# Kernel optimization log

Hardware: AMD Instinct MI355X
Metric: run time of the kernel (lower is better)

## Reference

```python
import jax, jax.numpy as jnp
import numpy as np

S = 2        # downscale
REDUCE = 32  # QK channel dim


def _to_grid(x):
    # [B,C,H,W] -> [B,C,H/S,W/S,S*S], matching ConverToGrid (reshape+permute+reshape)
    B, C, H, W = x.shape
    h, w = H // S, W // S
    x = x.reshape(B, C, h, S, w, S)
    x = x.transpose(0, 1, 2, 4, 3, 5)
    return x.reshape(B, C, h, w, S * S)


def setup_inputs() -> dict:
    key = jax.random.key(0)
    k1, k2, k3 = jax.random.split(key, 3)
    fm = jax.random.normal(k1, (8, 128, 256, 256), dtype=jnp.float32)
    Wq = jax.random.normal(k2, (REDUCE, 128), dtype=jnp.float32) * 0.05
    Wk = jax.random.normal(k3, (REDUCE, 128), dtype=jnp.float32) * 0.05
    return {"fm": fm, "Wq": Wq, "Wk": Wk}


def reference(fm, Wq, Wk):
    B, C, H, W = fm.shape
    h, w = H // S, W // S
    # Q branch: AvgPool2d(S,S) -> 1x1 conv -> scale by 1/sqrt(reduce)
    pooled = fm.reshape(B, C, h, S, w, S).mean(axis=(3, 5))          # [B,C,h,w]
    Q = jnp.einsum('rc,bchw->brhw', Wq, pooled) / jnp.sqrt(
        jnp.asarray(REDUCE, fm.dtype))                               # [B,r,h,w]
    # K branch: 1x1 conv -> grid
    K = _to_grid(jnp.einsum('rc,bchw->brhw', Wk, fm))                # [B,r,h,w,S*S]
    # V branch: grid of raw features
    V = _to_grid(fm)                                                 # [B,C,h,w,S*S]
    # sum over channel dim of Q*K, softmax over window dim (dropout p=0 => identity)
    logits = jnp.einsum('brhw,brhws->bhws', Q, K)                    # [B,h,w,S*S]
    attn = jax.nn.softmax(logits, axis=-1)
    # weighted sum over window positions
    out = jnp.einsum('bchws,bhws->bchw', V, attn)                    # [B,C,h,w]
    return out
```

## Files before the change

kernel.cpp:

```cpp
#include <hip/hip_runtime.h>
#include <hip/hip_bf16.h>
#include <math.h>


typedef unsigned int uint32;

__device__ __forceinline__ uint32 pack2(float x, float y) {
  union { __hip_bfloat162 h; uint32 u; } cvt;
  cvt.h = __float22bfloat162_rn(make_float2(x, y));
  return cvt.u;
}
__device__ __forceinline__ float2 unpack2(uint32 u) {
  float2 r;
  r.x = __uint_as_float(u << 16);
  r.y = __uint_as_float(u & 0xffff0000u);
  return r;
}

__global__ __launch_bounds__(256) void wt_kernel(const float* __restrict__ Wq,
                                                 const float* __restrict__ Wk,
                                                 float* __restrict__ ws) {
  int t = blockIdx.x * 256 + threadIdx.x;
  if (t < 4096) {
    int c = t >> 5, r = t & 31;
    ws[c * 32 + r]        = Wq[r * 128 + c] * (0.25f / sqrtf(32.0f));
    ws[4096 + c * 32 + r] = Wk[r * 128 + c];
  }
}

__global__ __launch_bounds__(256)
__attribute__((amdgpu_waves_per_eu(4, 4)))
void attn_main(const float* __restrict__ fm,
               const float* __restrict__ ws,
               float* __restrict__ out) {
  __shared__ float Qpart[2 * 32 * 64];
  __shared__ float lbuf[4 * 64 * 4];

  const int tid = threadIdx.x;
  const int p   = tid & 63;
  const int grp = __builtin_amdgcn_readfirstlane(tid >> 6);

  const int blk = blockIdx.x;
  const int w0  = (blk & 1) * 64;
  const int h   = (blk >> 1) & 127;
  const int b   = blk >> 8;
  const int cb  = grp * 32;

  const float* gbase = fm + ((size_t)(b * 128 + cb) * 65536) +
                       (size_t)(2 * h) * 256 + 2 * (w0 + p);
  const float* wq = ws + cb * 32;
  const float* wk = ws + 4096 + cb * 32;

  uint32 pka[32], pkb[32];
  {
    const float* g = gbase;
#pragma unroll
    for (int i = 0; i < 32; ++i) {
      const float2 va = *(const float2*)(g);
      const float2 vb = *(const float2*)(g + 256);
      pka[i] = pack2(va.x, va.y);
      pkb[i] = pack2(vb.x, vb.y);
      g += 65536;
    }
  }

  float qa[32];
#pragma unroll
  for (int r = 0; r < 32; ++r) qa[r] = 0.f;
#pragma unroll
  for (int i = 0; i < 32; ++i) {
    const float2 va = unpack2(pka[i]);
    const float2 vb = unpack2(pkb[i]);
    const float u = (va.x + va.y) + (vb.x + vb.y);
#pragma unroll
    for (int r = 0; r < 32; ++r)
      qa[r] = fmaf(wq[i * 32 + r], u, qa[r]);
  }

  if (grp >= 2) {
#pragma unroll
    for (int r = 0; r < 32; ++r) Qpart[(grp - 2) * 2048 + r * 64 + p] = qa[r];
  }
  __syncthreads();
  if (grp < 2) {
#pragma unroll
    for (int r = 0; r < 32; ++r) Qpart[grp * 2048 + r * 64 + p] += qa[r];
  }
  __syncthreads();
#pragma unroll
  for (int r = 0; r < 32; ++r)
    qa[r] = Qpart[r * 64 + p] + Qpart[2048 + r * 64 + p];

  float l0 = 0.f, l1 = 0.f, l2 = 0.f, l3 = 0.f;
#pragma unroll
  for (int i = 0; i < 32; ++i) {
    const float2 va = unpack2(pka[i]);
    const float2 vb = unpack2(pkb[i]);
    float t0 = 0.f, t1 = 0.f;
#pragma unroll
    for (int r = 0; r < 32; r += 2) {
      t0 = fmaf(qa[r + 0], wk[i * 32 + r + 0], t0);
      t1 = fmaf(qa[r + 1], wk[i * 32 + r + 1], t1);
    }
    const float tv = t0 + t1;
    l0 = fmaf(tv, va.x, l0);
    l1 = fmaf(tv, va.y, l1);
    l2 = fmaf(tv, vb.x, l2);
    l3 = fmaf(tv, vb.y, l3);
  }
  *(float4*)(lbuf + (grp * 64 + p) * 4) = make_float4(l0, l1, l2, l3);
  __syncthreads();

  if (grp == 0) {
    const float4 o1 = *(const float4*)(lbuf + (64 + p) * 4);
    const float4 o2 = *(const float4*)(lbuf + (128 + p) * 4);
    const float4 o3 = *(const float4*)(lbuf + (192 + p) * 4);
    const float L0 = (l0 + o1.x) + (o2.x + o3.x);
    const float L1 = (l1 + o1.y) + (o2.y + o3.y);
    const float L2 = (l2 + o1.z) + (o2.z + o3.z);
    const float L3 = (l3 + o1.w) + (o2.w + o3.w);
    const float mx = fmaxf(fmaxf(L0, L1), fmaxf(L2, L3));
    const float e0 = __expf(L0 - mx), e1 = __expf(L1 - mx);
    const float e2 = __expf(L2 - mx), e3 = __expf(L3 - mx);
    const float inv = 1.0f / ((e0 + e1) + (e2 + e3));
    *(float4*)(lbuf + p * 4) =
        make_float4(e0 * inv, e1 * inv, e2 * inv, e3 * inv);
  }
  __syncthreads();
  const float4 at = *(const float4*)(lbuf + p * 4);

  {
    float* op = out + ((size_t)(b * 128 + cb) * 16384) + h * 128 + w0 + p;
#pragma unroll
    for (int i = 0; i < 32; ++i) {
      const float2 va = unpack2(pka[i]);
      const float2 vb = unpack2(pkb[i]);
      op[(size_t)i * 16384] =
          fmaf(at.x, va.x, fmaf(at.y, va.y, fmaf(at.z, vb.x, at.w * vb.y)));
    }
  }
}

extern "C" void kernel_launch(void* const* d_in, const int* in_sizes, int n_in,
                              void* d_out, int out_size, void* d_ws, size_t ws_size,
                              hipStream_t stream) {
  const float* fm = (const float*)d_in[0];
  const float* Wq = (const float*)d_in[1];
  const float* Wk = (const float*)d_in[2];
  float* outp = (float*)d_out;
  float* ws = (float*)d_ws;

  wt_kernel<<<16, 256, 0, stream>>>(Wq, Wk, ws);
  attn_main<<<2048, 256, 0, stream>>>(fm, ws, outp);
}
```

Before: 168.8 us.

## Split channels across eight wavefronts per block instead of four

Each 64-pixel block now uses 512 threads, and each wavefront handles 16 channels instead of 32. This halves the per-thread register footprint for packed features and doubles in-flight loads per block. In exchange it adds an extra stage to the shared-memory Q reduction, uses more LDS, and removes the waves_per_eu hint. The aim is more memory-level parallelism and occupancy on this bandwidth-bound kernel.

```diff
diff --git a/kernel.cpp b/kernel.cpp
--- a/kernel.cpp
+++ b/kernel.cpp
@@ -28,39 +28,39 @@
   }
 }
 
-__global__ __launch_bounds__(256)
-__attribute__((amdgpu_waves_per_eu(4, 4)))
+__global__ __launch_bounds__(512)
 void attn_main(const float* __restrict__ fm,
                const float* __restrict__ ws,
                float* __restrict__ out) {
-  __shared__ float Qpart[2 * 32 * 64];
-  __shared__ float lbuf[4 * 64 * 4];
+  __shared__ float Qpart[4 * 32 * 64];
+  __shared__ float lbuf[8 * 64 * 4];
+  __shared__ float abuf[64 * 4];
 
   const int tid = threadIdx.x;
   const int p   = tid & 63;
-  const int grp = __builtin_amdgcn_readfirstlane(tid >> 6);
+  const int g   = __builtin_amdgcn_readfirstlane(tid >> 6);
 
   const int blk = blockIdx.x;
   const int w0  = (blk & 1) * 64;
   const int h   = (blk >> 1) & 127;
   const int b   = blk >> 8;
-  const int cb  = grp * 32;
+  const int cb  = g * 16;
 
   const float* gbase = fm + ((size_t)(b * 128 + cb) * 65536) +
                        (size_t)(2 * h) * 256 + 2 * (w0 + p);
   const float* wq = ws + cb * 32;
   const float* wk = ws + 4096 + cb * 32;
 
-  uint32 pka[32], pkb[32];
+  uint32 pka[16], pkb[16];
   {
-    const float* g = gbase;
+    const float* gp = gbase;
 #pragma unroll
-    for (int i = 0; i < 32; ++i) {
-      const float2 va = *(const float2*)(g);
-      const float2 vb = *(const float2*)(g + 256);
+    for (int i = 0; i < 16; ++i) {
+      const float2 va = *(const float2*)(gp);
+      const float2 vb = *(const float2*)(gp + 256);
       pka[i] = pack2(va.x, va.y);
       pkb[i] = pack2(vb.x, vb.y);
-      g += 65536;
+      gp += 65536;
     }
   }
 
@@ -68,7 +68,7 @@
 #pragma unroll
   for (int r = 0; r < 32; ++r) qa[r] = 0.f;
 #pragma unroll
-  for (int i = 0; i < 32; ++i) {
+  for (int i = 0; i < 16; ++i) {
     const float2 va = unpack2(pka[i]);
     const float2 vb = unpack2(pkb[i]);
     const float u = (va.x + va.y) + (vb.x + vb.y);
@@ -77,14 +77,20 @@
       qa[r] = fmaf(wq[i * 32 + r], u, qa[r]);
   }
 
-  if (grp >= 2) {
+  if (g >= 4) {
 #pragma unroll
-    for (int r = 0; r < 32; ++r) Qpart[(grp - 2) * 2048 + r * 64 + p] = qa[r];
+    for (int r = 0; r < 32; ++r) Qpart[(g - 4) * 2048 + r * 64 + p] = qa[r];
   }
   __syncthreads();
-  if (grp < 2) {
+  if (g < 4) {
 #pragma unroll
-    for (int r = 0; r < 32; ++r) Qpart[grp * 2048 + r * 64 + p] += qa[r];
+    for (int r = 0; r < 32; ++r) Qpart[g * 2048 + r * 64 + p] += qa[r];
+  }
+  __syncthreads();
+  if (g < 2) {
+#pragma unroll
+    for (int r = 0; r < 32; ++r)
+      Qpart[g * 2048 + r * 64 + p] += Qpart[(g + 2) * 2048 + r * 64 + p];
   }
   __syncthreads();
 #pragma unroll
@@ -93,7 +99,7 @@
 
   float l0 = 0.f, l1 = 0.f, l2 = 0.f, l3 = 0.f;
 #pragma unroll
-  for (int i = 0; i < 32; ++i) {
+  for (int i = 0; i < 16; ++i) {
     const float2 va = unpack2(pka[i]);
     const float2 vb = unpack2(pkb[i]);
     float t0 = 0.f, t1 = 0.f;
@@ -108,31 +114,30 @@
     l2 = fmaf(tv, vb.x, l2);
     l3 = fmaf(tv, vb.y, l3);
   }
-  *(float4*)(lbuf + (grp * 64 + p) * 4) = make_float4(l0, l1, l2, l3);
+  *(float4*)(lbuf + (g * 64 + p) * 4) = make_float4(l0, l1, l2, l3);
   __syncthreads();
 
-  if (grp == 0) {
-    const float4 o1 = *(const float4*)(lbuf + (64 + p) * 4);
-    const float4 o2 = *(const float4*)(lbuf + (128 + p) * 4);
-    const float4 o3 = *(const float4*)(lbuf + (192 + p) * 4);
-    const float L0 = (l0 + o1.x) + (o2.x + o3.x);
-    const float L1 = (l1 + o1.y) + (o2.y + o3.y);
-    const float L2 = (l2 + o1.z) + (o2.z + o3.z);
-    const float L3 = (l3 + o1.w) + (o2.w + o3.w);
+  if (tid < 64) {
+    float L0 = 0.f, L1 = 0.f, L2 = 0.f, L3 = 0.f;
+#pragma unroll
+    for (int k = 0; k < 8; ++k) {
+      const float4 s = *(const float4*)(lbuf + (k * 64 + tid) * 4);
+      L0 += s.x; L1 += s.y; L2 += s.z; L3 += s.w;
+    }
     const float mx = fmaxf(fmaxf(L0, L1), fmaxf(L2, L3));
     const float e0 = __expf(L0 - mx), e1 = __expf(L1 - mx);
     const float e2 = __expf(L2 - mx), e3 = __expf(L3 - mx);
     const float inv = 1.0f / ((e0 + e1) + (e2 + e3));
-    *(float4*)(lbuf + p * 4) =
+    *(float4*)(abuf + tid * 4) =
         make_float4(e0 * inv, e1 * inv, e2 * inv, e3 * inv);
   }
   __syncthreads();
-  const float4 at = *(const float4*)(lbuf + p * 4);
+  const float4 at = *(const float4*)(abuf + p * 4);
 
   {
     float* op = out + ((size_t)(b * 128 + cb) * 16384) + h * 128 + w0 + p;
 #pragma unroll
-    for (int i = 0; i < 32; ++i) {
+    for (int i = 0; i < 16; ++i) {
       const float2 va = unpack2(pka[i]);
       const float2 vb = unpack2(pkb[i]);
       op[(size_t)i * 16384] =
@@ -151,5 +156,5 @@
   float* ws = (float*)d_ws;
 
   wt_kernel<<<16, 256, 0, stream>>>(Wq, Wk, ws);
-  attn_main<<<2048, 256, 0, stream>>>(fm, ws, outp);
+  attn_main<<<2048, 512, 0, stream>>>(fm, ws, outp);
 }
```

New measurement: 138.3 us. 18.1% less time.

## Split QK reduction dim across waves and stash packed features in LDS

Applied to the files above, without the earlier changes.

Each wave now owns 8 of the 32 reduced channels and streams all 128 input channels, computing Q and K per window position directly and producing partial logits. That replaces the cross-wave Q reduction through LDS and the second pass over packed registers. Raw features are stored as packed bf16 in a shared stash for the output pass, with a software prefetch of the next 8 channels, and the fixed waves-per-EU attribute is dropped. The cost is that every wave loads the full channel stack, so the same global data is read four times through the cache. The FMA count per thread and the redundant LDS writes also go up.

```diff
diff --git a/kernel.cpp b/kernel.cpp
--- a/kernel.cpp
+++ b/kernel.cpp
@@ -29,112 +29,108 @@
 }
 
 __global__ __launch_bounds__(256)
-__attribute__((amdgpu_waves_per_eu(4, 4)))
 void attn_main(const float* __restrict__ fm,
                const float* __restrict__ ws,
                float* __restrict__ out) {
-  __shared__ float Qpart[2 * 32 * 64];
-  __shared__ float lbuf[4 * 64 * 4];
+  __shared__ uint2 stash[128][64];
+  __shared__ float lbuf[4][64][4];
+  __shared__ float abuf[64][4];
 
   const int tid = threadIdx.x;
   const int p   = tid & 63;
-  const int grp = __builtin_amdgcn_readfirstlane(tid >> 6);
+  const int w   = __builtin_amdgcn_readfirstlane(tid >> 6);
 
   const int blk = blockIdx.x;
   const int w0  = (blk & 1) * 64;
   const int h   = (blk >> 1) & 127;
   const int b   = blk >> 8;
-  const int cb  = grp * 32;
 
-  const float* gbase = fm + ((size_t)(b * 128 + cb) * 65536) +
-                       (size_t)(2 * h) * 256 + 2 * (w0 + p);
-  const float* wq = ws + cb * 32;
-  const float* wk = ws + 4096 + cb * 32;
+  const float* g = fm + ((size_t)(b * 128)) * 65536 +
+                   (size_t)(2 * h) * 256 + 2 * (w0 + p);
+  const float* wq = ws + 8 * w;
+  const float* wk = ws + 4096 + 8 * w;
 
-  uint32 pka[32], pkb[32];
-  {
-    const float* g = gbase;
+  float Kacc[8][4];
+  float Qacc[8];
 #pragma unroll
-    for (int i = 0; i < 32; ++i) {
-      const float2 va = *(const float2*)(g);
-      const float2 vb = *(const float2*)(g + 256);
-      pka[i] = pack2(va.x, va.y);
-      pkb[i] = pack2(vb.x, vb.y);
-      g += 65536;
+  for (int r = 0; r < 8; ++r) {
+    Qacc[r] = 0.f;
+    Kacc[r][0] = Kacc[r][1] = Kacc[r][2] = Kacc[r][3] = 0.f;
+  }
+
+  float2 ra[8], rb[8];
+#pragma unroll
+  for (int i = 0; i < 8; ++i) {
+    ra[i] = *(const float2*)(g + (size_t)i * 65536);
+    rb[i] = *(const float2*)(g + (size_t)i * 65536 + 256);
+  }
+
+  for (int c0 = 0; c0 < 128; c0 += 8) {
+    const bool pf = (c0 < 120);
+#pragma unroll
+    for (int j = 0; j < 8; ++j) {
+      const int c = c0 + j;
+      const float2 va = ra[j];
+      const float2 vb = rb[j];
+      if (pf) {
+        ra[j] = *(const float2*)(g + (size_t)(c + 8) * 65536);
+        rb[j] = *(const float2*)(g + (size_t)(c + 8) * 65536 + 256);
+      }
+      stash[c][p] = make_uint2(pack2(va.x, va.y), pack2(vb.x, vb.y));
+      const float u = (va.x + va.y) + (vb.x + vb.y);
+#pragma unroll
+      for (int r = 0; r < 8; ++r) {
+        const float wqv = wq[c * 32 + r];
+        const float wkv = wk[c * 32 + r];
+        Qacc[r] = fmaf(wqv, u, Qacc[r]);
+        Kacc[r][0] = fmaf(wkv, va.x, Kacc[r][0]);
+        Kacc[r][1] = fmaf(wkv, va.y, Kacc[r][1]);
+        Kacc[r][2] = fmaf(wkv, vb.x, Kacc[r][2]);
+        Kacc[r][3] = fmaf(wkv, vb.y, Kacc[r][3]);
+      }
     }
   }
 
-  float qa[32];
+  {
+    float pl0 = 0.f, pl1 = 0.f, pl2 = 0.f, pl3 = 0.f;
 #pragma unroll
-  for (int r = 0; r < 32; ++r) qa[r] = 0.f;
-#pragma unroll
-  for (int i = 0; i < 32; ++i) {
-    const float2 va = unpack2(pka[i]);
-    const float2 vb = unpack2(pkb[i]);
-    const float u = (va.x + va.y) + (vb.x + vb.y);
-#pragma unroll
-    for (int r = 0; r < 32; ++r)
-      qa[r] = fmaf(wq[i * 32 + r], u, qa[r]);
-  }
-
-  if (grp >= 2) {
-#pragma unroll
-    for (int r = 0; r < 32; ++r) Qpart[(grp - 2) * 2048 + r * 64 + p] = qa[r];
+    for (int r = 0; r < 8; ++r) {
+      pl0 = fmaf(Qacc[r], Kacc[r][0], pl0);
+      pl1 = fmaf(Qacc[r], Kacc[r][1], pl1);
+      pl2 = fmaf(Qacc[r], Kacc[r][2], pl2);
+      pl3 = fmaf(Qacc[r], Kacc[r][3], pl3);
+    }
+    *(float4*)&lbuf[w][p][0] = make_float4(pl0, pl1, pl2, pl3);
   }
   __syncthreads();
-  if (grp < 2) {
-#pragma unroll
-    for (int r = 0; r < 32; ++r) Qpart[grp * 2048 + r * 64 + p] += qa[r];
-  }
-  __syncthreads();
-#pragma unroll
-  for (int r = 0; r < 32; ++r)
-    qa[r] = Qpart[r * 64 + p] + Qpart[2048 + r * 64 + p];
 
-  float l0 = 0.f, l1 = 0.f, l2 = 0.f, l3 = 0.f;
-#pragma unroll
-  for (int i = 0; i < 32; ++i) {
-    const float2 va = unpack2(pka[i]);
-    const float2 vb = unpack2(pkb[i]);
-    float t0 = 0.f, t1 = 0.f;
-#pragma unroll
-    for (int r = 0; r < 32; r += 2) {
-      t0 = fmaf(qa[r + 0], wk[i * 32 + r + 0], t0);
-      t1 = fmaf(qa[r + 1], wk[i * 32 + r + 1], t1);
-    }
-    const float tv = t0 + t1;
-    l0 = fmaf(tv, va.x, l0);
-    l1 = fmaf(tv, va.y, l1);
-    l2 = fmaf(tv, vb.x, l2);
-    l3 = fmaf(tv, vb.y, l3);
-  }
-  *(float4*)(lbuf + (grp * 64 + p) * 4) = make_float4(l0, l1, l2, l3);
-  __syncthreads();
-
-  if (grp == 0) {
-    const float4 o1 = *(const float4*)(lbuf + (64 + p) * 4);
-    const float4 o2 = *(const float4*)(lbuf + (128 + p) * 4);
-    const float4 o3 = *(const float4*)(lbuf + (192 + p) * 4);
-    const float L0 = (l0 + o1.x) + (o2.x + o3.x);
-    const float L1 = (l1 + o1.y) + (o2.y + o3.y);
-    const float L2 = (l2 + o1.z) + (o2.z + o3.z);
-    const float L3 = (l3 + o1.w) + (o2.w + o3.w);
+  if (tid < 64) {
+    const float4 s0 = *(const float4*)&lbuf[0][tid][0];
+    const float4 s1 = *(const float4*)&lbuf[1][tid][0];
+    const float4 s2 = *(const float4*)&lbuf[2][tid][0];
+    const float4 s3 = *(const float4*)&lbuf[3][tid][0];
+    const float L0 = (s0.x + s1.x) + (s2.x + s3.x);
+    const float L1 = (s0.y + s1.y) + (s2.y + s3.y);
+    const float L2 = (s0.z + s1.z) + (s2.z + s3.z);
+    const float L3 = (s0.w + s1.w) + (s2.w + s3.w);
     const float mx = fmaxf(fmaxf(L0, L1), fmaxf(L2, L3));
     const float e0 = __expf(L0 - mx), e1 = __expf(L1 - mx);
     const float e2 = __expf(L2 - mx), e3 = __expf(L3 - mx);
     const float inv = 1.0f / ((e0 + e1) + (e2 + e3));
-    *(float4*)(lbuf + p * 4) =
+    *(float4*)&abuf[tid][0] =
         make_float4(e0 * inv, e1 * inv, e2 * inv, e3 * inv);
   }
   __syncthreads();
-  const float4 at = *(const float4*)(lbuf + p * 4);
 
   {
-    float* op = out + ((size_t)(b * 128 + cb) * 16384) + h * 128 + w0 + p;
-#pragma unroll
+    const float4 at = *(const float4*)&abuf[p][0];
+    const int cb = 32 * w;
+    float* op = out + ((size_t)(b * 128 + cb)) * 16384 + h * 128 + w0 + p;
+#pragma unroll 8
     for (int i = 0; i < 32; ++i) {
-      const float2 va = unpack2(pka[i]);
-      const float2 vb = unpack2(pkb[i]);
+      const uint2 q = stash[cb + i][p];
+      const float2 va = unpack2(q.x);
+      const float2 vb = unpack2(q.y);
       op[(size_t)i * 16384] =
           fmaf(at.x, va.x, fmaf(at.y, va.y, fmaf(at.z, vb.x, at.w * vb.y)));
     }
```

Result: faster. 146.8 us (-13.0%).
